# Kernel optimization log

Hardware: AMD Instinct MI355X
Metric: run time of the kernel (lower is better)

## Reference

```python
import jax, jax.numpy as jnp
import numpy as np

N = 50000
E = 600000
HIDDEN = 128
HEADS = 4
HEAD_DIM = HIDDEN // HEADS
NEG_SLOPE = 0.2
LN_EPS = 1e-5


def setup_inputs() -> dict:
    key = jax.random.key(0)
    ks = jax.random.split(key, 16)
    s = 1.0 / np.sqrt(HIDDEN)
    inp = {
        "h": jax.random.normal(ks[0], (N, HIDDEN), dtype=jnp.float32),
        "src": jax.random.randint(ks[1], (E,), 0, N, dtype=jnp.int32),
        "dst": jax.random.randint(ks[2], (E,), 0, N, dtype=jnp.int32),
        # GATv2 params (share_weights=False, bias=True)
        "W_src": jax.random.normal(ks[3], (HIDDEN, HIDDEN), dtype=jnp.float32) * s,
        "b_src": jnp.zeros((HIDDEN,), dtype=jnp.float32),
        "W_dst": jax.random.normal(ks[4], (HIDDEN, HIDDEN), dtype=jnp.float32) * s,
        "b_dst": jnp.zeros((HIDDEN,), dtype=jnp.float32),
        "attn": jax.random.normal(ks[5], (HEADS, HEAD_DIM), dtype=jnp.float32) * s,
        # FFN params
        "W1": jax.random.normal(ks[6], (HIDDEN, 2 * HIDDEN), dtype=jnp.float32) * s,
        "bf1": jnp.zeros((2 * HIDDEN,), dtype=jnp.float32),
        "W2": jax.random.normal(ks[7], (2 * HIDDEN, HIDDEN), dtype=jnp.float32) * (1.0 / np.sqrt(2 * HIDDEN)),
        "bf2": jnp.zeros((HIDDEN,), dtype=jnp.float32),
        # LayerNorms
        "g1": jnp.ones((HIDDEN,), dtype=jnp.float32),
        "beta1": jnp.zeros((HIDDEN,), dtype=jnp.float32),
        "g2": jnp.ones((HIDDEN,), dtype=jnp.float32),
        "beta2": jnp.zeros((HIDDEN,), dtype=jnp.float32),
    }
    return inp


def _layernorm(x, g, b):
    mu = jnp.mean(x, axis=-1, keepdims=True)
    var = jnp.mean(jnp.square(x - mu), axis=-1, keepdims=True)
    return (x - mu) * jax.lax.rsqrt(var + LN_EPS) * g + b


def reference(h, src, dst, W_src, b_src, W_dst, b_dst, attn,
              W1, bf1, W2, bf2, g1, beta1, g2, beta2):
    # --- GATv2 attention (eval mode, dropouts are identity) ---
    fs = (h @ W_src + b_src).reshape(N, HEADS, HEAD_DIM)   # [N,H,D]
    fd = (h @ W_dst + b_dst).reshape(N, HEADS, HEAD_DIM)
    e = jax.nn.leaky_relu(fs[src] + fd[dst], NEG_SLOPE)    # [E,H,D]
    logits = jnp.einsum('ehd,hd->eh', e, attn)             # [E,H]
    # edge softmax over incoming edges of each dst node
    m = jax.ops.segment_max(logits, dst, num_segments=N)   # [N,H]
    m = jnp.where(jnp.isfinite(m), m, 0.0)                 # guard zero-in-degree
    a = jnp.exp(logits - m[dst])                           # [E,H]
    denom = jax.ops.segment_sum(a, dst, num_segments=N)    # [N,H]
    denom = jnp.where(denom == 0.0, 1.0, denom)
    alpha = a / denom[dst]                                 # [E,H]
    msg = fs[src] * alpha[:, :, None]                      # [E,H,D]
    rst = jax.ops.segment_sum(msg, dst, num_segments=N)    # [N,H,D]
    h_attn = rst.reshape(N, HIDDEN)
    # --- residual + LN, FFN + residual + LN ---
    h1 = _layernorm(h + h_attn, g1, beta1)
    ffn = jax.nn.gelu(h1 @ W1 + bf1, approximate=False) @ W2 + bf2
    out = _layernorm(h1 + ffn, g2, beta2)
    return out
```

## Files before the change

kernel.cpp:

```cpp
#include <hip/hip_runtime.h>
#include <math.h>

#define N_NODES 50000
#define N_EDGES 600000
#define HID 128
#define FFN_HID 256
#define NEG_SLOPE 0.2f
#define LN_EPS 1e-5f
#define BKT 64

typedef unsigned short u16;
typedef unsigned int u32;
typedef __attribute__((ext_vector_type(8))) short short8;
typedef __attribute__((ext_vector_type(4))) float floatx4;

__device__ __forceinline__ u16 f2bf(float x) {
    unsigned int u = __float_as_uint(x);
    unsigned int r = u + 0x7FFFu + ((u >> 16) & 1u);
    return (u16)(r >> 16);
}
__device__ __forceinline__ float bf2f(u16 x) {
    return __uint_as_float(((unsigned int)x) << 16);
}


__global__ void scatter_bucket(const int* __restrict__ src, const int* __restrict__ dst,
                               int* __restrict__ cursor, int* __restrict__ ebkt) {
    int e = blockIdx.x * blockDim.x + threadIdx.x;
    if (e < N_EDGES) {
        int d = dst[e];
        int slot = atomicAdd(&cursor[d], 1);
        if (slot < BKT) ebkt[(size_t)d * BKT + slot] = src[e];
    }
}


__global__ void prep_all(const float* __restrict__ Wsrc, const float* __restrict__ Wdst,
                         const float* __restrict__ W1, const float* __restrict__ W2,
                         u16* __restrict__ B1, u16* __restrict__ B2, u16* __restrict__ B3) {
    int t = blockIdx.x * blockDim.x + threadIdx.x;
    const float* W; u16* out; int K, Nc, noff;
    if (t < 16384)       { W = Wsrc; out = B1; K = 128; Nc = 128; noff = 0; }
    else if (t < 32768)  { W = Wdst; out = B1; K = 128; Nc = 128; noff = 128; t -= 16384; }
    else if (t < 65536)  { W = W1;   out = B2; K = 128; Nc = 256; noff = 0;   t -= 32768; }
    else if (t < 98304)  { W = W2;   out = B3; K = 256; Nc = 128; noff = 0;   t -= 65536; }
    else return;
    int n = t % Nc, k = t / Nc;
    int ng = noff + n;
    int ksteps = K >> 5;
    int frag = (ng >> 4) * ksteps + (k >> 5);
    int lane = ((k >> 3) & 3) * 16 + (ng & 15);
    int j = k & 7;
    out[((size_t)frag * 64 + lane) * 8 + j] = f2bf(W[(size_t)k * Nc + n]);
}


__global__ __launch_bounds__(256) void gemm_fsfd_mfma(
    const float* __restrict__ h, const u16* __restrict__ Bsw,
    const float* __restrict__ bsrc, const float* __restrict__ bdst,
    u16* __restrict__ fsb, u16* __restrict__ fdb)
{
    int tid = threadIdx.x, wave = tid >> 6, lane = tid & 63;
    int lrow = lane & 15, lq = lane >> 4;
    short8 bfrag[4][4];
    #pragma unroll
    for (int nt = 0; nt < 4; nt++)
        #pragma unroll
        for (int ks = 0; ks < 4; ks++) {
            int frag = (wave * 4 + nt) * 4 + ks;
            bfrag[nt][ks] = *(const short8*)(Bsw + ((size_t)frag * 64 + lane) * 8);
        }
    float bias[4];
    #pragma unroll
    for (int nt = 0; nt < 4; nt++) {
        int cg = wave * 64 + nt * 16 + lrow;
        bias[nt] = (cg < HID) ? bsrc[cg] : bdst[cg - HID];
    }
    for (int mb = blockIdx.x; mb < N_NODES / 16; mb += gridDim.x) {
        int m0 = mb * 16;
        const float* hrow = h + (size_t)(m0 + lrow) * HID;
        floatx4 acc[4];
        #pragma unroll
        for (int nt = 0; nt < 4; nt++) acc[nt] = {0.f, 0.f, 0.f, 0.f};
        #pragma unroll
        for (int ks = 0; ks < 4; ks++) {
            float4 va = *(const float4*)(hrow + ks * 32 + lq * 8);
            float4 vb = *(const float4*)(hrow + ks * 32 + lq * 8 + 4);
            short8 a;
            a[0] = (short)f2bf(va.x); a[1] = (short)f2bf(va.y);
            a[2] = (short)f2bf(va.z); a[3] = (short)f2bf(va.w);
            a[4] = (short)f2bf(vb.x); a[5] = (short)f2bf(vb.y);
            a[6] = (short)f2bf(vb.z); a[7] = (short)f2bf(vb.w);
            #pragma unroll
            for (int nt = 0; nt < 4; nt++)
                acc[nt] = __builtin_amdgcn_mfma_f32_16x16x32_bf16(a, bfrag[nt][ks], acc[nt], 0, 0, 0);
        }
        #pragma unroll
        for (int nt = 0; nt < 4; nt++) {
            int cg = wave * 64 + nt * 16 + lrow;
            u16* outp = (cg < HID) ? (fsb + cg) : (fdb + cg - HID);
            #pragma unroll
            for (int r = 0; r < 4; r++) {
                int row = m0 + lq * 4 + r;
                outp[(size_t)row * HID] = f2bf(acc[nt][r] + bias[nt]);
            }
        }
    }
}


__global__ __launch_bounds__(256) void aggregate_kernel(
    const u16* __restrict__ fsb, const u16* __restrict__ fdb,
    const float* __restrict__ h, const float* __restrict__ attn,
    const int* __restrict__ counts, const int* __restrict__ ebkt,
    const float* __restrict__ g1, const float* __restrict__ beta1,
    u16* __restrict__ h1b)
{
    int wave = threadIdx.x >> 6, lane = threadIdx.x & 63;
    int node = blockIdx.x * 4 + wave;
    if (node >= N_NODES) return;
    int half = lane >> 5, sub = lane & 31;
    int f = sub * 4;

    uint2 ud = *(const uint2*)&fdb[(size_t)node * HID + f];
    float fd0 = bf2f((u16)(ud.x & 0xffff)), fd1 = bf2f((u16)(ud.x >> 16));
    float fd2 = bf2f((u16)(ud.y & 0xffff)), fd3 = bf2f((u16)(ud.y >> 16));
    float4 a4 = *(const float4*)&attn[f];
    float c10 = 0.6f * a4.x, c20 = 0.4f * a4.x;
    float c11 = 0.6f * a4.y, c21 = 0.4f * a4.y;
    float c12 = 0.6f * a4.z, c22 = 0.4f * a4.z;
    float c13 = 0.6f * a4.w, c23 = 0.4f * a4.w;

    int cnt = counts[node];
    const int* brow = ebkt + (size_t)node * BKT;
    float acc0 = 0.f, acc1 = 0.f, acc2 = 0.f, acc3 = 0.f, lsum = 0.f;

    auto body = [&](int e) {
        int s = brow[e];
        uint2 u = *(const uint2*)&fsb[(size_t)s * HID + f];
        float x0 = bf2f((u16)(u.x & 0xffff)), x1 = bf2f((u16)(u.x >> 16));
        float x2 = bf2f((u16)(u.y & 0xffff)), x3 = bf2f((u16)(u.y >> 16));
        float e0 = x0 + fd0, e1 = x1 + fd1, e2 = x2 + fd2, e3 = x3 + fd3;
        float p = c10 * e0 + c20 * fabsf(e0);
        p += c11 * e1 + c21 * fabsf(e1);
        p += c12 * e2 + c22 * fabsf(e2);
        p += c13 * e3 + c23 * fabsf(e3);
        p += __shfl_xor(p, 1); p += __shfl_xor(p, 2); p += __shfl_xor(p, 4);
        float w = __expf(p);
        lsum += w;
        acc0 += w * x0; acc1 += w * x1; acc2 += w * x2; acc3 += w * x3;
    };

    int e = half;
    for (; e + 2 < cnt; e += 4) { body(e); body(e + 2); }
    for (; e < cnt; e += 2) body(e);

    acc0 += __shfl_xor(acc0, 32); acc1 += __shfl_xor(acc1, 32);
    acc2 += __shfl_xor(acc2, 32); acc3 += __shfl_xor(acc3, 32);
    lsum += __shfl_xor(lsum, 32);

    float inv = (lsum > 0.f) ? (1.0f / lsum) : 0.f;
    float4 hh = *(const float4*)&h[(size_t)node * HID + f];
    float o0 = hh.x + acc0 * inv, o1 = hh.y + acc1 * inv;
    float o2 = hh.z + acc2 * inv, o3 = hh.w + acc3 * inv;
    float s1 = (o0 + o1) + (o2 + o3);
    float s2 = (o0 * o0 + o1 * o1) + (o2 * o2 + o3 * o3);
    #pragma unroll
    for (int mk = 1; mk < 32; mk <<= 1) { s1 += __shfl_xor(s1, mk); s2 += __shfl_xor(s2, mk); }
    float mu = s1 * (1.0f / HID);
    float var = s2 * (1.0f / HID) - mu * mu;
    float rs = rsqrtf(var + LN_EPS);
    if (half == 0) {
        float4 gv = *(const float4*)&g1[f], bv = *(const float4*)&beta1[f];
        ushort4 ob;
        ob.x = f2bf((o0 - mu) * rs * gv.x + bv.x);
        ob.y = f2bf((o1 - mu) * rs * gv.y + bv.y);
        ob.z = f2bf((o2 - mu) * rs * gv.z + bv.z);
        ob.w = f2bf((o3 - mu) * rs * gv.w + bv.w);
        *(ushort4*)&h1b[(size_t)node * HID + f] = ob;
    }
}


#define TS_PAD 8

__global__ __launch_bounds__(256) void ffn_fused(
    const u16* __restrict__ h1b, const u16* __restrict__ B2sw, const u16* __restrict__ B3sw,
    const float* __restrict__ bf1, const float* __restrict__ bf2,
    const float* __restrict__ g2, const float* __restrict__ beta2,
    float* __restrict__ out)
{
    __shared__ u16 ts[16][FFN_HID + TS_PAD];
    __shared__ float xs[16][HID];
    int tid = threadIdx.x, wave = tid >> 6, lane = tid & 63;
    int lrow = lane & 15, lq = lane >> 4;

    short8 b1f[4][4];
    #pragma unroll
    for (int nt = 0; nt < 4; nt++)
        #pragma unroll
        for (int ks = 0; ks < 4; ks++) {
            int frag = (wave * 4 + nt) * 4 + ks;
            b1f[nt][ks] = *(const short8*)(B2sw + ((size_t)frag * 64 + lane) * 8);
        }
    short8 b2f[2][8];
    #pragma unroll
    for (int nt = 0; nt < 2; nt++)
        #pragma unroll
        for (int ks = 0; ks < 8; ks++) {
            int frag = (wave * 2 + nt) * 8 + ks;
            b2f[nt][ks] = *(const short8*)(B3sw + ((size_t)frag * 64 + lane) * 8);
        }
    float bias1[4];
    #pragma unroll
    for (int nt = 0; nt < 4; nt++) bias1[nt] = bf1[wave * 64 + nt * 16 + lrow];
    float bias2[2];
    #pragma unroll
    for (int nt = 0; nt < 2; nt++) bias2[nt] = bf2[wave * 32 + nt * 16 + lrow];

    for (int mb = blockIdx.x; mb < N_NODES / 16; mb += gridDim.x) {
        int m0 = mb * 16;
        floatx4 acc1[4];
        #pragma unroll
        for (int nt = 0; nt < 4; nt++) acc1[nt] = {0.f, 0.f, 0.f, 0.f};
        #pragma unroll
        for (int ks = 0; ks < 4; ks++) {
            short8 a = *(const short8*)(h1b + (size_t)(m0 + lrow) * HID + ks * 32 + lq * 8);
            #pragma unroll
            for (int nt = 0; nt < 4; nt++)
                acc1[nt] = __builtin_amdgcn_mfma_f32_16x16x32_bf16(a, b1f[nt][ks], acc1[nt], 0, 0, 0);
        }
        #pragma unroll
        for (int nt = 0; nt < 4; nt++) {
            int cg = wave * 64 + nt * 16 + lrow;
            #pragma unroll
            for (int r = 0; r < 4; r++) {
                float v = acc1[nt][r] + bias1[nt];
                float ge = v * 0.5f * (1.0f + erff(v * 0.70710678118654752440f));
                ts[lq * 4 + r][cg] = f2bf(ge);
            }
        }
        __syncthreads();
        floatx4 acc2[2];
        #pragma unroll
        for (int nt = 0; nt < 2; nt++) acc2[nt] = {0.f, 0.f, 0.f, 0.f};
        #pragma unroll
        for (int ks = 0; ks < 8; ks++) {
            short8 a = *(const short8*)&ts[lrow][ks * 32 + lq * 8];
            #pragma unroll
            for (int nt = 0; nt < 2; nt++)
                acc2[nt] = __builtin_amdgcn_mfma_f32_16x16x32_bf16(a, b2f[nt][ks], acc2[nt], 0, 0, 0);
        }
        #pragma unroll
        for (int nt = 0; nt < 2; nt++) {
            int cg = wave * 32 + nt * 16 + lrow;
            #pragma unroll
            for (int r = 0; r < 4; r++) {
                int row = m0 + lq * 4 + r;
                float resid = bf2f(h1b[(size_t)row * HID + cg]);
                xs[lq * 4 + r][cg] = acc2[nt][r] + bias2[nt] + resid;
            }
        }
        __syncthreads();
        int row = tid >> 4, c0 = (tid & 15) * 8;
        float v[8];
        float s1 = 0.f, s2 = 0.f;
        #pragma unroll
        for (int i = 0; i < 8; i++) { v[i] = xs[row][c0 + i]; s1 += v[i]; s2 += v[i] * v[i]; }
        s1 += __shfl_xor(s1, 1); s2 += __shfl_xor(s2, 1);
        s1 += __shfl_xor(s1, 2); s2 += __shfl_xor(s2, 2);
        s1 += __shfl_xor(s1, 4); s2 += __shfl_xor(s2, 4);
        s1 += __shfl_xor(s1, 8); s2 += __shfl_xor(s2, 8);
        float mu = s1 * (1.0f / HID);
        float var = s2 * (1.0f / HID) - mu * mu;
        float rs = rsqrtf(var + LN_EPS);
        float o[8];
        #pragma unroll
        for (int i = 0; i < 8; i++) o[i] = (v[i] - mu) * rs * g2[c0 + i] + beta2[c0 + i];
        float* op = out + (size_t)(m0 + row) * HID + c0;
        *(float4*)(op)     = make_float4(o[0], o[1], o[2], o[3]);
        *(float4*)(op + 4) = make_float4(o[4], o[5], o[6], o[7]);
        __syncthreads();
    }
}


extern "C" void kernel_launch(void* const* d_in, const int* in_sizes, int n_in,
                              void* d_out, int out_size, void* d_ws, size_t ws_size,
                              hipStream_t stream)
{
    const float* h    = (const float*)d_in[0];
    const int*   src  = (const int*)d_in[1];
    const int*   dst  = (const int*)d_in[2];
    const float* Wsrc = (const float*)d_in[3];
    const float* bsrc = (const float*)d_in[4];
    const float* Wdst = (const float*)d_in[5];
    const float* bdst = (const float*)d_in[6];
    const float* attn = (const float*)d_in[7];
    const float* W1   = (const float*)d_in[8];
    const float* bf1  = (const float*)d_in[9];
    const float* W2   = (const float*)d_in[10];
    const float* bf2  = (const float*)d_in[11];
    const float* g1   = (const float*)d_in[12];
    const float* beta1= (const float*)d_in[13];
    const float* g2   = (const float*)d_in[14];
    const float* beta2= (const float*)d_in[15];
    float* out = (float*)d_out;

    u16* fsb = (u16*)d_ws;
    u16* fdb = fsb + (size_t)N_NODES * HID;
    u16* h1b = fdb + (size_t)N_NODES * HID;
    u16* B1 = h1b + (size_t)N_NODES * HID;
    u16* B2 = B1 + 32768;
    u16* B3 = B2 + 32768;
    int* cursor = (int*)(B3 + 32768);
    int* ebkt   = cursor + N_NODES;

    hipMemsetAsync(cursor, 0, N_NODES * sizeof(int), stream);
    scatter_bucket<<<(N_EDGES + 255) / 256, 256, 0, stream>>>(src, dst, cursor, ebkt);
    prep_all<<<384, 256, 0, stream>>>(Wsrc, Wdst, W1, W2, B1, B2, B3);

    gemm_fsfd_mfma<<<N_NODES / 16, 256, 0, stream>>>(h, B1, bsrc, bdst, fsb, fdb);
    aggregate_kernel<<<(N_NODES + 3) / 4, 256, 0, stream>>>(fsb, fdb, h, attn, cursor, ebkt, g1, beta1, h1b);
    ffn_fused<<<N_NODES / 16, 256, 0, stream>>>(h1b, B2, B3, bf1, bf2, g2, beta2, out);
}
```

Before: 238.0 us.

## Merge prep kernels, shrink edge buckets to u16, widen aggregate loads, bf16 residual

```diff
diff --git a/kernel.cpp b/kernel.cpp
--- a/kernel.cpp
+++ b/kernel.cpp
@@ -19,26 +19,29 @@
     unsigned int r = u + 0x7FFFu + ((u >> 16) & 1u);
     return (u16)(r >> 16);
 }
-__device__ __forceinline__ float bf2f(u16 x) {
-    return __uint_as_float(((unsigned int)x) << 16);
-}
-
-
-__global__ void scatter_bucket(const int* __restrict__ src, const int* __restrict__ dst,
-                               int* __restrict__ cursor, int* __restrict__ ebkt) {
-    int e = blockIdx.x * blockDim.x + threadIdx.x;
-    if (e < N_EDGES) {
-        int d = dst[e];
-        int slot = atomicAdd(&cursor[d], 1);
-        if (slot < BKT) ebkt[(size_t)d * BKT + slot] = src[e];
-    }
-}
-
-
-__global__ void prep_all(const float* __restrict__ Wsrc, const float* __restrict__ Wdst,
-                         const float* __restrict__ W1, const float* __restrict__ W2,
-                         u16* __restrict__ B1, u16* __restrict__ B2, u16* __restrict__ B3) {
-    int t = blockIdx.x * blockDim.x + threadIdx.x;
+__device__ __forceinline__ float bflo(u32 u) { return __uint_as_float(u << 16); }
+__device__ __forceinline__ float bfhi(u32 u) { return __uint_as_float(u & 0xffff0000u); }
+__device__ __forceinline__ u32 packbf(float lo, float hi) {
+    return (u32)f2bf(lo) | ((u32)f2bf(hi) << 16);
+}
+
+
+__global__ void scatter_prep(const int* __restrict__ src, const int* __restrict__ dst,
+                             int* __restrict__ cursor, u16* __restrict__ ebkt,
+                             const float* __restrict__ Wsrc, const float* __restrict__ Wdst,
+                             const float* __restrict__ W1, const float* __restrict__ W2,
+                             u16* __restrict__ B1, u16* __restrict__ B2, u16* __restrict__ B3) {
+    int b = blockIdx.x;
+    if (b < 2344) {
+        int e = b * 256 + threadIdx.x;
+        if (e < N_EDGES) {
+            int d = dst[e];
+            int slot = atomicAdd(&cursor[d], 1);
+            if (slot < BKT) ebkt[(size_t)d * BKT + slot] = (u16)src[e];
+        }
+        return;
+    }
+    int t = (b - 2344) * 256 + threadIdx.x;
     const float* W; u16* out; int K, Nc, noff;
     if (t < 16384)       { W = Wsrc; out = B1; K = 128; Nc = 128; noff = 0; }
     else if (t < 32768)  { W = Wdst; out = B1; K = 128; Nc = 128; noff = 128; t -= 16384; }
@@ -58,7 +61,7 @@
 __global__ __launch_bounds__(256) void gemm_fsfd_mfma(
     const float* __restrict__ h, const u16* __restrict__ Bsw,
     const float* __restrict__ bsrc, const float* __restrict__ bdst,
-    u16* __restrict__ fsb, u16* __restrict__ fdb)
+    u16* __restrict__ fsb, u16* __restrict__ fdb, u16* __restrict__ hb)
 {
     int tid = threadIdx.x, wave = tid >> 6, lane = tid & 63;
     int lrow = lane & 15, lq = lane >> 4;
@@ -91,6 +94,8 @@
             a[2] = (short)f2bf(va.z); a[3] = (short)f2bf(va.w);
             a[4] = (short)f2bf(vb.x); a[5] = (short)f2bf(vb.y);
             a[6] = (short)f2bf(vb.z); a[7] = (short)f2bf(vb.w);
+            if (wave == 0)
+                *(short8*)(hb + (size_t)(m0 + lrow) * HID + ks * 32 + lq * 8) = a;
             #pragma unroll
             for (int nt = 0; nt < 4; nt++)
                 acc[nt] = __builtin_amdgcn_mfma_f32_16x16x32_bf16(a, bfrag[nt][ks], acc[nt], 0, 0, 0);
@@ -111,73 +116,90 @@
 
 __global__ __launch_bounds__(256) void aggregate_kernel(
     const u16* __restrict__ fsb, const u16* __restrict__ fdb,
-    const float* __restrict__ h, const float* __restrict__ attn,
-    const int* __restrict__ counts, const int* __restrict__ ebkt,
+    const u16* __restrict__ hb, const float* __restrict__ attn,
+    const int* __restrict__ counts, const u16* __restrict__ ebkt,
     const float* __restrict__ g1, const float* __restrict__ beta1,
     u16* __restrict__ h1b)
 {
     int wave = threadIdx.x >> 6, lane = threadIdx.x & 63;
     int node = blockIdx.x * 4 + wave;
     if (node >= N_NODES) return;
-    int half = lane >> 5, sub = lane & 31;
-    int f = sub * 4;
-
-    uint2 ud = *(const uint2*)&fdb[(size_t)node * HID + f];
-    float fd0 = bf2f((u16)(ud.x & 0xffff)), fd1 = bf2f((u16)(ud.x >> 16));
-    float fd2 = bf2f((u16)(ud.y & 0xffff)), fd3 = bf2f((u16)(ud.y >> 16));
-    float4 a4 = *(const float4*)&attn[f];
-    float c10 = 0.6f * a4.x, c20 = 0.4f * a4.x;
-    float c11 = 0.6f * a4.y, c21 = 0.4f * a4.y;
-    float c12 = 0.6f * a4.z, c22 = 0.4f * a4.z;
-    float c13 = 0.6f * a4.w, c23 = 0.4f * a4.w;
-
-    int cnt = counts[node];
-    const int* brow = ebkt + (size_t)node * BKT;
-    float acc0 = 0.f, acc1 = 0.f, acc2 = 0.f, acc3 = 0.f, lsum = 0.f;
+    int grp = lane >> 4, fl = lane & 15;
+    int f = fl * 8;
+
+    uint4 ud = *(const uint4*)&fdb[(size_t)node * HID + f];
+    float fdv[8] = { bflo(ud.x), bfhi(ud.x), bflo(ud.y), bfhi(ud.y),
+                     bflo(ud.z), bfhi(ud.z), bflo(ud.w), bfhi(ud.w) };
+    float4 aA = *(const float4*)&attn[f];
+    float4 aB = *(const float4*)&attn[f + 4];
+    float c1[8] = { 0.6f * aA.x, 0.6f * aA.y, 0.6f * aA.z, 0.6f * aA.w,
+                    0.6f * aB.x, 0.6f * aB.y, 0.6f * aB.z, 0.6f * aB.w };
+    float c2[8] = { 0.4f * aA.x, 0.4f * aA.y, 0.4f * aA.z, 0.4f * aA.w,
+                    0.4f * aB.x, 0.4f * aB.y, 0.4f * aB.z, 0.4f * aB.w };
+
+    int cnt = counts[node]; cnt = cnt < BKT ? cnt : BKT;
+    const u16* brow = ebkt + (size_t)node * BKT;
+    float acc[8] = {0.f, 0.f, 0.f, 0.f, 0.f, 0.f, 0.f, 0.f};
+    float lsum = 0.f;
 
     auto body = [&](int e) {
-        int s = brow[e];
-        uint2 u = *(const uint2*)&fsb[(size_t)s * HID + f];
-        float x0 = bf2f((u16)(u.x & 0xffff)), x1 = bf2f((u16)(u.x >> 16));
-        float x2 = bf2f((u16)(u.y & 0xffff)), x3 = bf2f((u16)(u.y >> 16));
-        float e0 = x0 + fd0, e1 = x1 + fd1, e2 = x2 + fd2, e3 = x3 + fd3;
-        float p = c10 * e0 + c20 * fabsf(e0);
-        p += c11 * e1 + c21 * fabsf(e1);
-        p += c12 * e2 + c22 * fabsf(e2);
-        p += c13 * e3 + c23 * fabsf(e3);
-        p += __shfl_xor(p, 1); p += __shfl_xor(p, 2); p += __shfl_xor(p, 4);
+        int s = (int)brow[e];
+        uint4 u = *(const uint4*)&fsb[(size_t)s * HID + f];
+        float x[8] = { bflo(u.x), bfhi(u.x), bflo(u.y), bfhi(u.y),
+                       bflo(u.z), bfhi(u.z), bflo(u.w), bfhi(u.w) };
+        float p = 0.f;
+        #pragma unroll
+        for (int i = 0; i < 8; i++) {
+            float ei = x[i] + fdv[i];
+            p = fmaf(c1[i], ei, p);
+            p = fmaf(c2[i], fabsf(ei), p);
+        }
+        p += __shfl_xor(p, 1); p += __shfl_xor(p, 2);
         float w = __expf(p);
         lsum += w;
-        acc0 += w * x0; acc1 += w * x1; acc2 += w * x2; acc3 += w * x3;
+        #pragma unroll
+        for (int i = 0; i < 8; i++) acc[i] = fmaf(w, x[i], acc[i]);
     };
 
-    int e = half;
-    for (; e + 2 < cnt; e += 4) { body(e); body(e + 2); }
-    for (; e < cnt; e += 2) body(e);
-
-    acc0 += __shfl_xor(acc0, 32); acc1 += __shfl_xor(acc1, 32);
-    acc2 += __shfl_xor(acc2, 32); acc3 += __shfl_xor(acc3, 32);
-    lsum += __shfl_xor(lsum, 32);
+    int e = grp;
+    for (; e + 4 < cnt; e += 8) { body(e); body(e + 4); }
+    if (e < cnt) body(e);
+
+    #pragma unroll
+    for (int i = 0; i < 8; i++) {
+        acc[i] += __shfl_xor(acc[i], 16);
+        acc[i] += __shfl_xor(acc[i], 32);
+    }
+    lsum += __shfl_xor(lsum, 16); lsum += __shfl_xor(lsum, 32);
 
     float inv = (lsum > 0.f) ? (1.0f / lsum) : 0.f;
-    float4 hh = *(const float4*)&h[(size_t)node * HID + f];
-    float o0 = hh.x + acc0 * inv, o1 = hh.y + acc1 * inv;
-    float o2 = hh.z + acc2 * inv, o3 = hh.w + acc3 * inv;
-    float s1 = (o0 + o1) + (o2 + o3);
-    float s2 = (o0 * o0 + o1 * o1) + (o2 * o2 + o3 * o3);
-    #pragma unroll
-    for (int mk = 1; mk < 32; mk <<= 1) { s1 += __shfl_xor(s1, mk); s2 += __shfl_xor(s2, mk); }
+    uint4 uh = *(const uint4*)&hb[(size_t)node * HID + f];
+    float hx[8] = { bflo(uh.x), bfhi(uh.x), bflo(uh.y), bfhi(uh.y),
+                    bflo(uh.z), bfhi(uh.z), bflo(uh.w), bfhi(uh.w) };
+    float o[8], s1 = 0.f, s2 = 0.f;
+    #pragma unroll
+    for (int i = 0; i < 8; i++) {
+        o[i] = hx[i] + acc[i] * inv;
+        s1 += o[i]; s2 += o[i] * o[i];
+    }
+    s1 += __shfl_xor(s1, 1); s2 += __shfl_xor(s2, 1);
+    s1 += __shfl_xor(s1, 2); s2 += __shfl_xor(s2, 2);
+    s1 += __shfl_xor(s1, 4); s2 += __shfl_xor(s2, 4);
+    s1 += __shfl_xor(s1, 8); s2 += __shfl_xor(s2, 8);
     float mu = s1 * (1.0f / HID);
     float var = s2 * (1.0f / HID) - mu * mu;
     float rs = rsqrtf(var + LN_EPS);
-    if (half == 0) {
-        float4 gv = *(const float4*)&g1[f], bv = *(const float4*)&beta1[f];
-        ushort4 ob;
-        ob.x = f2bf((o0 - mu) * rs * gv.x + bv.x);
-        ob.y = f2bf((o1 - mu) * rs * gv.y + bv.y);
-        ob.z = f2bf((o2 - mu) * rs * gv.z + bv.z);
-        ob.w = f2bf((o3 - mu) * rs * gv.w + bv.w);
-        *(ushort4*)&h1b[(size_t)node * HID + f] = ob;
+    if (grp == 0) {
+        float4 gA = *(const float4*)&g1[f], gB = *(const float4*)&g1[f + 4];
+        float4 bA = *(const float4*)&beta1[f], bB = *(const float4*)&beta1[f + 4];
+        float q0 = (o[0] - mu) * rs * gA.x + bA.x, q1 = (o[1] - mu) * rs * gA.y + bA.y;
+        float q2 = (o[2] - mu) * rs * gA.z + bA.z, q3 = (o[3] - mu) * rs * gA.w + bA.w;
+        float q4 = (o[4] - mu) * rs * gB.x + bB.x, q5 = (o[5] - mu) * rs * gB.y + bB.y;
+        float q6 = (o[6] - mu) * rs * gB.z + bB.z, q7 = (o[7] - mu) * rs * gB.w + bB.w;
+        uint4 ob;
+        ob.x = packbf(q0, q1); ob.y = packbf(q2, q3);
+        ob.z = packbf(q4, q5); ob.w = packbf(q6, q7);
+        *(uint4*)&h1b[(size_t)node * HID + f] = ob;
     }
 }
 
@@ -257,7 +279,8 @@
             #pragma unroll
             for (int r = 0; r < 4; r++) {
                 int row = m0 + lq * 4 + r;
-                float resid = bf2f(h1b[(size_t)row * HID + cg]);
+                float resid = bflo((u32)h1b[(size_t)row * HID + cg] << 0) ;
+                resid = __uint_as_float(((u32)h1b[(size_t)row * HID + cg]) << 16);
                 xs[lq * 4 + r][cg] = acc2[nt][r] + bias2[nt] + resid;
             }
         }
@@ -310,17 +333,17 @@
     u16* fsb = (u16*)d_ws;
     u16* fdb = fsb + (size_t)N_NODES * HID;
     u16* h1b = fdb + (size_t)N_NODES * HID;
-    u16* B1 = h1b + (size_t)N_NODES * HID;
+    u16* hb  = h1b + (size_t)N_NODES * HID;
+    u16* B1 = hb + (size_t)N_NODES * HID;
     u16* B2 = B1 + 32768;
     u16* B3 = B2 + 32768;
     int* cursor = (int*)(B3 + 32768);
-    int* ebkt   = cursor + N_NODES;
+    u16* ebkt   = (u16*)(cursor + N_NODES);
 
     hipMemsetAsync(cursor, 0, N_NODES * sizeof(int), stream);
-    scatter_bucket<<<(N_EDGES + 255) / 256, 256, 0, stream>>>(src, dst, cursor, ebkt);
-    prep_all<<<384, 256, 0, stream>>>(Wsrc, Wdst, W1, W2, B1, B2, B3);
-
-    gemm_fsfd_mfma<<<N_NODES / 16, 256, 0, stream>>>(h, B1, bsrc, bdst, fsb, fdb);
-    aggregate_kernel<<<(N_NODES + 3) / 4, 256, 0, stream>>>(fsb, fdb, h, attn, cursor, ebkt, g1, beta1, h1b);
-    ffn_fused<<<N_NODES / 16, 256, 0, stream>>>(h1b, B2, B3, bf1, bf2, g2, beta2, out);
-}
+    scatter_prep<<<2728, 256, 0, stream>>>(src, dst, cursor, ebkt,
+                                           Wsrc, Wdst, W1, W2, B1, B2, B3);
+    gemm_fsfd_mfma<<<1024, 256, 0, stream>>>(h, B1, bsrc, bdst, fsb, fdb, hb);
+    aggregate_kernel<<<(N_NODES + 3) / 4, 256, 0, stream>>>(fsb, fdb, hb, attn, cursor, ebkt, g1, beta1, h1b);
+    ffn_fused<<<640, 256, 0, stream>>>(h1b, B2, B3, bf1, bf2, g2, beta2, out);
+}
```

Result: faster. 228.7 us (-3.9%).
